# Optimization experiments

Hardware: AMD Instinct MI355X
Metric: run time of the kernel (lower is better)

The kernel has to match this reference:

```python
import jax, jax.numpy as jnp
import numpy as np


def setup_inputs() -> dict:
    key = jax.random.key(0)
    B, T, D, H = 64, 512, 1024, 1024
    ks = jax.random.split(key, 14)
    s = 1.0 / np.sqrt(D)  # torch nn.Linear init scale
    u = lambda k, shape: jax.random.uniform(k, shape, jnp.float32, -s, s)
    return {
        "x": jax.random.normal(ks[0], (B, T, D), jnp.float32),
        "h0": jnp.zeros((B, 1, H), jnp.float32),
        "Wfz": u(ks[1], (H, D)), "bfz": u(ks[2], (H,)),
        "Wfr": u(ks[3], (H, D)), "bfr": u(ks[4], (H,)),
        "Wfh": u(ks[5], (H, D)), "bfh": u(ks[6], (H,)),
        "Wuz": u(ks[7], (H, H)), "buz": u(ks[8], (H,)),
        "Wur": u(ks[9], (H, H)), "bur": u(ks[10], (H,)),
        "Wuh": u(ks[11], (H, H)), "buh": u(ks[12], (H,)),
        "chunk_size": 1,
    }


def reference(x, h0, Wfz, bfz, Wfr, bfr, Wfh, bfh, Wuz, buz, Wur, bur, Wuh, buh, chunk_size):
    # Input-side projections are time-independent: batch them over the whole
    # sequence (same math as applying fz/fr/fh per step).
    Xz = x @ Wfz.T + bfz  # [B,T,H]
    Xr = x @ Wfr.T + bfr
    Xh = x @ Wfh.T + bfh

    def step(h, xs):  # h: [B,H]
        xz, xr, xh = xs
        z = jax.nn.sigmoid(xz + h @ Wuz.T + buz)
        r = jax.nn.sigmoid(xr + h @ Wur.T + bur)
        h_hat = jax.nn.silu(xh + (r * h) @ Wuh.T + buh)
        h = (1.0 - z) * h + z * h_hat
        return h, h

    xs = (Xz.transpose(1, 0, 2), Xr.transpose(1, 0, 2), Xh.transpose(1, 0, 2))  # [T,B,H]
    h_last, ys = jax.lax.scan(step, h0[:, 0, :], xs)
    y = ys.transpose(1, 0, 2)  # [B,T,H]
    return y, h_last[:, None, :]
```

## Files before the change

### kernel.cpp

```cpp
#include <hip/hip_runtime.h>
#include <hip/hip_bf16.h>

typedef short s16x8 __attribute__((ext_vector_type(8)));
typedef float f32x4 __attribute__((ext_vector_type(4)));

__device__ __forceinline__ float bf2f(unsigned short s) {
  union { unsigned int u; float f; } c; c.u = ((unsigned int)s) << 16; return c.f;
}
__device__ __forceinline__ short f2bf(float f) {
  union { float f; unsigned int u; } c; c.f = f;
  unsigned int r = (c.u + 0x7fffu + ((c.u >> 16) & 1u)) >> 16;
  return (short)(unsigned short)r;
}
__device__ __forceinline__ float sigm(float x) { return 1.0f / (1.0f + __expf(-x)); }

__device__ __forceinline__ void gload_lds16(const short* g, short* l) {
  __builtin_amdgcn_global_load_lds((const __attribute__((address_space(1))) void*)g,
                                   (__attribute__((address_space(3))) void*)l, 16, 0, 0);
}

__device__ __forceinline__ void cload8(const short* p,
    s16x8& d0, s16x8& d1, s16x8& d2, s16x8& d3,
    s16x8& d4, s16x8& d5, s16x8& d6, s16x8& d7)
{
  asm volatile(
    "global_load_dwordx4 %0, %[p], off sc0 sc1\n\t"
    "global_load_dwordx4 %1, %[p], off offset:64 sc0 sc1\n\t"
    "global_load_dwordx4 %2, %[p], off offset:128 sc0 sc1\n\t"
    "global_load_dwordx4 %3, %[p], off offset:192 sc0 sc1\n\t"
    "global_load_dwordx4 %4, %[p], off offset:256 sc0 sc1\n\t"
    "global_load_dwordx4 %5, %[p], off offset:320 sc0 sc1\n\t"
    "global_load_dwordx4 %6, %[p], off offset:384 sc0 sc1\n\t"
    "global_load_dwordx4 %7, %[p], off offset:448 sc0 sc1"
    : "=&v"(d0), "=&v"(d1), "=&v"(d2), "=&v"(d3),
      "=&v"(d4), "=&v"(d5), "=&v"(d6), "=&v"(d7)
    : [p]"v"(p) : "memory");
}

__global__ void prep(const float* __restrict__ x,
                     const float* __restrict__ Wfz, const float* __restrict__ Wfr, const float* __restrict__ Wfh,
                     const float* __restrict__ Wuz, const float* __restrict__ Wur, const float* __restrict__ Wuh,
                     const float* __restrict__ h0,
                     short* __restrict__ xb, short* __restrict__ Wf, short* __restrict__ Wzr,
                     short* __restrict__ Wh, short* __restrict__ hb)
{
  const long NX = 33554432L;
  const long NW = 1048576L;
  const long TOT = NX + 6*NW + 65536L;
  long stride = (long)gridDim.x * blockDim.x;
  for (long p = (long)blockIdx.x * blockDim.x + threadIdx.x; p < TOT; p += stride) {
    if (p < NX) { xb[p] = f2bf(x[p]); }
    else if (p < NX + 3*NW) {
      long q = p - NX;
      float v = q < NW ? Wfz[q] : (q < 2*NW ? Wfr[q-NW] : Wfh[q-2*NW]);
      Wf[q] = f2bf(v);
    } else if (p < NX + 5*NW) {
      long q = p - NX - 3*NW;
      float v = q < NW ? Wuz[q] : Wur[q-NW];
      Wzr[q] = f2bf(v);
    } else if (p < NX + 6*NW) {
      long q = p - NX - 5*NW;
      Wh[q] = f2bf(Wuh[q]);
    } else {
      long q = p - NX - 6*NW;
      hb[q] = f2bf(h0[q]);
    }
  }
}

__global__ __launch_bounds__(256) void gemm_x(const short* __restrict__ A, const short* __restrict__ Bw,
    const float* __restrict__ bfz, const float* __restrict__ bfr, const float* __restrict__ bfh,
    short* __restrict__ X)
{
  constexpr int M = 32768, K = 1024;
  constexpr int BM = 128, BN = 128, BK = 32;
  __shared__ __align__(16) short As[BM*BK];
  __shared__ __align__(16) short Bs[BN*BK];
  int tid = threadIdx.x, lane = tid & 63, wid = tid >> 6;
  int bm = blockIdx.x % (M/BM), bn = blockIdx.x / (M/BM);
  int wm = wid >> 1, wn = wid & 1;

  f32x4 acc[4][4];
  for (int i = 0; i < 4; ++i) for (int j = 0; j < 4; ++j) acc[i][j] = f32x4{0.f,0.f,0.f,0.f};

  int r0 = tid >> 2,        kc0 = (tid & 3) * 8;
  int r1 = (256+tid) >> 2,  kc1 = ((256+tid) & 3) * 8;
  const short* a0 = A  + (size_t)(bm*BM + r0)*K + kc0;
  const short* a1 = A  + (size_t)(bm*BM + r1)*K + kc1;
  const short* b0 = Bw + (size_t)(bn*BN + r0)*K + kc0;
  const short* b1 = Bw + (size_t)(bn*BN + r1)*K + kc1;

  const short* abase = As + (wm*64 + (lane&15))*BK + (lane>>4)*8;
  const short* bbase = Bs + (wn*64 + (lane&15))*BK + (lane>>4)*8;

  for (int k0 = 0; k0 < K; k0 += BK) {
    __syncthreads();
    gload_lds16(a0 + k0, As + wid*512);
    gload_lds16(a1 + k0, As + 2048 + wid*512);
    gload_lds16(b0 + k0, Bs + wid*512);
    gload_lds16(b1 + k0, Bs + 2048 + wid*512);
    __syncthreads();
    s16x8 af[4], bff[4];
    for (int f = 0; f < 4; ++f) {
      af[f]  = *(const s16x8*)(abase + f*16*BK);
      bff[f] = *(const s16x8*)(bbase + f*16*BK);
    }
    for (int i = 0; i < 4; ++i)
      for (int j = 0; j < 4; ++j)
        acc[i][j] = __builtin_amdgcn_mfma_f32_16x16x32_bf16(af[i], bff[j], acc[i][j], 0, 0, 0);
  }

  int col = lane & 15, rb = (lane >> 4) * 4;
  for (int fi = 0; fi < 4; ++fi) for (int fj = 0; fj < 4; ++fj) {
    int n = bn*BN + wn*64 + fj*16 + col;
    float bias = n < 1024 ? bfz[n] : (n < 2048 ? bfr[n-1024] : bfh[n-2048]);
    f32x4 c = acc[fi][fj];
    for (int i = 0; i < 4; ++i) {
      int m = bm*BM + wm*64 + fi*16 + rb + i;
      int bb = m >> 9, tt = m & 511;
      X[((size_t)tt*64 + bb)*3072 + n] = f2bf(c[i] + bias);
    }
  }
}

#define WAITV(N) asm volatile("s_waitcnt vmcnt(" #N ")" ::: "memory"); \
                 __builtin_amdgcn_sched_barrier(0);

__global__ __launch_bounds__(64, 1) void recur(
  const short* __restrict__ X,
  const short* __restrict__ Wzr,
  const short* __restrict__ Wh,
  const float* __restrict__ h0,
  const float* __restrict__ buz, const float* __restrict__ bur, const float* __restrict__ buh,
  short* hb,
  short* rh,
  float* y, float* hlast, int* bar)
{
  __shared__ __align__(16) short Wl[3*32*64*8];

  int wg = blockIdx.x;
  int cg = wg & 63, bg = wg >> 6;
  int lane = threadIdx.x;
  int col = lane & 15, hi = lane >> 4;
  int rb = hi*4, kfo = hi*8;
  int j  = cg*16 + col;
  int b0 = bg*16 + rb;
  int arow = bg*16 + col;

  {
    const short* gbase0 = Wzr + (size_t)(cg*16 + col)*1024 + kfo;
    const short* gbase1 = Wzr + (size_t)(1024 + cg*16 + col)*1024 + kfo;
    const short* gbase2 = Wh  + (size_t)(cg*16 + col)*1024 + kfo;
    #pragma unroll 4
    for (int n = 0; n < 32; ++n) {
      *(s16x8*)(Wl + ((0*32+n)*64 + lane)*8) = *(const s16x8*)(gbase0 + n*32);
      *(s16x8*)(Wl + ((1*32+n)*64 + lane)*8) = *(const s16x8*)(gbase1 + n*32);
      *(s16x8*)(Wl + ((2*32+n)*64 + lane)*8) = *(const s16x8*)(gbase2 + n*32);
    }
  }

  float bz = buz[j], br = bur[j], bh = buh[j];
  float hreg[4], zreg[4];
  #pragma unroll
  for (int i = 0; i < 4; ++i) hreg[i] = h0[(b0+i)*1024 + j];

  unsigned short xs[12], xn[12];
  #pragma unroll
  for (int i = 0; i < 4; ++i) {
    const unsigned short* xp = (const unsigned short*)X + ((size_t)(b0+i))*3072 + j;
    xs[i] = xp[0]; xs[4+i] = xp[1024]; xs[8+i] = xp[2048];
  }

  const short* wlbase = Wl + lane*8;
  int* cnt = bar + bg*64;
  int tgt = 64;

  asm volatile("s_waitcnt vmcnt(0)" ::: "memory");

  for (int t = 0; t < 512; ++t) {
    const short* hbc = hb + (t&1)*65536;
    short* hbn = hb + ((t&1)^1)*65536;

    {
      const short* ap = hbc + (size_t)arow*1024 + kfo;
      s16x8 ah[32];
      cload8(ap,     ah[0], ah[1], ah[2], ah[3], ah[4], ah[5], ah[6], ah[7]);
      cload8(ap+256, ah[8], ah[9], ah[10],ah[11],ah[12],ah[13],ah[14],ah[15]);
      cload8(ap+512, ah[16],ah[17],ah[18],ah[19],ah[20],ah[21],ah[22],ah[23]);
      cload8(ap+768, ah[24],ah[25],ah[26],ah[27],ah[28],ah[29],ah[30],ah[31]);
      f32x4 acz = {0.f,0.f,0.f,0.f}, acr = {0.f,0.f,0.f,0.f};
      WAITV(24)
      #pragma unroll
      for (int n = 0; n < 8; ++n) {
        s16x8 vz = *(const s16x8*)(wlbase + n*512);
        s16x8 vr = *(const s16x8*)(wlbase + 16384 + n*512);
        acz = __builtin_amdgcn_mfma_f32_16x16x32_bf16(ah[n], vz, acz, 0,0,0);
        acr = __builtin_amdgcn_mfma_f32_16x16x32_bf16(ah[n], vr, acr, 0,0,0);
      }
      WAITV(16)
      #pragma unroll
      for (int n = 8; n < 16; ++n) {
        s16x8 vz = *(const s16x8*)(wlbase + n*512);
        s16x8 vr = *(const s16x8*)(wlbase + 16384 + n*512);
        acz = __builtin_amdgcn_mfma_f32_16x16x32_bf16(ah[n], vz, acz, 0,0,0);
        acr = __builtin_amdgcn_mfma_f32_16x16x32_bf16(ah[n], vr, acr, 0,0,0);
      }
      WAITV(8)
      #pragma unroll
      for (int n = 16; n < 24; ++n) {
        s16x8 vz = *(const s16x8*)(wlbase + n*512);
        s16x8 vr = *(const s16x8*)(wlbase + 16384 + n*512);
        acz = __builtin_amdgcn_mfma_f32_16x16x32_bf16(ah[n], vz, acz, 0,0,0);
        acr = __builtin_amdgcn_mfma_f32_16x16x32_bf16(ah[n], vr, acr, 0,0,0);
      }
      WAITV(0)
      #pragma unroll
      for (int n = 24; n < 32; ++n) {
        s16x8 vz = *(const s16x8*)(wlbase + n*512);
        s16x8 vr = *(const s16x8*)(wlbase + 16384 + n*512);
        acz = __builtin_amdgcn_mfma_f32_16x16x32_bf16(ah[n], vz, acz, 0,0,0);
        acr = __builtin_amdgcn_mfma_f32_16x16x32_bf16(ah[n], vr, acr, 0,0,0);
      }
      #pragma unroll
      for (int i = 0; i < 4; ++i) {
        zreg[i] = sigm(bf2f(xs[i]) + acz[i] + bz);
        float r = sigm(bf2f(xs[4+i]) + acr[i] + br);
        __hip_atomic_store(rh + (b0+i)*1024 + j, f2bf(r * hreg[i]),
                           __ATOMIC_RELAXED, __HIP_MEMORY_SCOPE_AGENT);
      }
    }
    asm volatile("s_waitcnt vmcnt(0)" ::: "memory");
    if (lane == 0)
      __hip_atomic_fetch_add(cnt, 1, __ATOMIC_RELAXED, __HIP_MEMORY_SCOPE_AGENT);
    {
      int v;
      do { v = __hip_atomic_load(cnt, __ATOMIC_RELAXED, __HIP_MEMORY_SCOPE_AGENT); }
      while (v < tgt);
      tgt += 64;
    }

    {
      const short* ap = rh + (size_t)arow*1024 + kfo;
      s16x8 ah[32];
      cload8(ap,     ah[0], ah[1], ah[2], ah[3], ah[4], ah[5], ah[6], ah[7]);
      cload8(ap+256, ah[8], ah[9], ah[10],ah[11],ah[12],ah[13],ah[14],ah[15]);
      cload8(ap+512, ah[16],ah[17],ah[18],ah[19],ah[20],ah[21],ah[22],ah[23]);
      cload8(ap+768, ah[24],ah[25],ah[26],ah[27],ah[28],ah[29],ah[30],ah[31]);
      f32x4 ach = {0.f,0.f,0.f,0.f};
      WAITV(24)
      #pragma unroll
      for (int n = 0; n < 8; ++n) {
        s16x8 vh = *(const s16x8*)(wlbase + 32768 + n*512);
        ach = __builtin_amdgcn_mfma_f32_16x16x32_bf16(ah[n], vh, ach, 0,0,0);
      }
      WAITV(16)
      #pragma unroll
      for (int n = 8; n < 16; ++n) {
        s16x8 vh = *(const s16x8*)(wlbase + 32768 + n*512);
        ach = __builtin_amdgcn_mfma_f32_16x16x32_bf16(ah[n], vh, ach, 0,0,0);
      }
      WAITV(8)
      #pragma unroll
      for (int n = 16; n < 24; ++n) {
        s16x8 vh = *(const s16x8*)(wlbase + 32768 + n*512);
        ach = __builtin_amdgcn_mfma_f32_16x16x32_bf16(ah[n], vh, ach, 0,0,0);
      }
      WAITV(0)
      #pragma unroll
      for (int n = 24; n < 32; ++n) {
        s16x8 vh = *(const s16x8*)(wlbase + 32768 + n*512);
        ach = __builtin_amdgcn_mfma_f32_16x16x32_bf16(ah[n], vh, ach, 0,0,0);
      }
      float hnv[4];
      #pragma unroll
      for (int i = 0; i < 4; ++i) {
        float s  = bf2f(xs[8+i]) + ach[i] + bh;
        float hh = s * sigm(s);
        float hn = (1.0f - zreg[i])*hreg[i] + zreg[i]*hh;
        hnv[i] = hn; hreg[i] = hn;
        __hip_atomic_store(hbn + (b0+i)*1024 + j, f2bf(hn),
                           __ATOMIC_RELAXED, __HIP_MEMORY_SCOPE_AGENT);
      }
      asm volatile("s_waitcnt vmcnt(0)" ::: "memory");
      if (lane == 0)
        __hip_atomic_fetch_add(cnt, 1, __ATOMIC_RELAXED, __HIP_MEMORY_SCOPE_AGENT);
      #pragma unroll
      for (int i = 0; i < 4; ++i)
        __builtin_nontemporal_store(hnv[i], y + ((size_t)(b0+i)*512 + t)*1024 + j);
      int tn = (t+1) & 511;
      #pragma unroll
      for (int i = 0; i < 4; ++i) {
        const unsigned short* xp = (const unsigned short*)X + ((size_t)tn*64 + (b0+i))*3072 + j;
        xn[i] = xp[0]; xn[4+i] = xp[1024]; xn[8+i] = xp[2048];
      }
      if (t == 511) {
        #pragma unroll
        for (int i = 0; i < 4; ++i) hlast[(b0+i)*1024 + j] = hreg[i];
      }
      {
        int v;
        do { v = __hip_atomic_load(cnt, __ATOMIC_RELAXED, __HIP_MEMORY_SCOPE_AGENT); }
        while (v < tgt);
        tgt += 64;
      }
    }

    #pragma unroll
    for (int q = 0; q < 12; ++q) xs[q] = xn[q];
  }
}

extern "C" void kernel_launch(void* const* d_in, const int* in_sizes, int n_in,
                              void* d_out, int out_size, void* d_ws, size_t ws_size,
                              hipStream_t stream) {
  const float* x   = (const float*)d_in[0];
  const float* h0  = (const float*)d_in[1];
  const float* Wfz = (const float*)d_in[2];
  const float* bfz = (const float*)d_in[3];
  const float* Wfr = (const float*)d_in[4];
  const float* bfr = (const float*)d_in[5];
  const float* Wfh = (const float*)d_in[6];
  const float* bfh = (const float*)d_in[7];
  const float* Wuz = (const float*)d_in[8];
  const float* buz = (const float*)d_in[9];
  const float* Wur = (const float*)d_in[10];
  const float* bur = (const float*)d_in[11];
  const float* Wuh = (const float*)d_in[12];
  const float* buh = (const float*)d_in[13];

  char* ws = (char*)d_ws;
  short* Xb  = (short*)(ws);
  short* xb  = (short*)(ws + 201326592);
  short* Wf  = (short*)(ws + 268435456);
  short* Wzr = (short*)(ws + 274726912);
  short* Wh  = (short*)(ws + 278921216);
  short* hb  = (short*)(ws + 281018368);
  short* rh  = (short*)(ws + 281280512);
  int*   bar = (int*)(ws + 281411584);

  float* y = (float*)d_out;
  float* hlast = y + 33554432;

  hipMemsetAsync(bar, 0, 1024, stream);
  prep<<<2048, 256, 0, stream>>>(x, Wfz, Wfr, Wfh, Wuz, Wur, Wuh, h0, xb, Wf, Wzr, Wh, hb);
  gemm_x<<<6144, 256, 0, stream>>>(xb, Wf, bfz, bfr, bfh, Xb);
  recur<<<256, 64, 0, stream>>>(Xb, Wzr, Wh, h0, buz, bur, buh, hb, rh, y, hlast, bar);
}
```

Before: 3.808 ms.

## Split recurrence into compute and helper waves, defer z-gate MFMAs past barrier

The recurrent kernel now runs two waves per block. A helper wave prefetches the X projections into LDS two steps ahead and writes y outputs from an LDS staging buffer, which takes global stores and loads off the critical wave. The compute wave computes r first, publishes r*h, and spreads the z-gate MFMAs across the grid barrier so they overlap the wait. It also uses split accumulators to shorten MFMA dependency chains and a multi-outstanding-load barrier poll. In exchange it adds intra-block flag handshakes that can stall the compute wave, plus extra ordering complexity.

```diff
diff --git a/kernel.cpp b/kernel.cpp
--- a/kernel.cpp
+++ b/kernel.cpp
@@ -18,6 +18,9 @@
   __builtin_amdgcn_global_load_lds((const __attribute__((address_space(1))) void*)g,
                                    (__attribute__((address_space(3))) void*)l, 16, 0, 0);
 }
+
+#define SB() __builtin_amdgcn_sched_barrier(0)
+#define WAITV(N) asm volatile("s_waitcnt vmcnt(" #N ")" ::: "memory"); SB();
 
 __device__ __forceinline__ void cload8(const short* p,
     s16x8& d0, s16x8& d1, s16x8& d2, s16x8& d3,
@@ -35,6 +38,38 @@
     : "=&v"(d0), "=&v"(d1), "=&v"(d2), "=&v"(d3),
       "=&v"(d4), "=&v"(d5), "=&v"(d6), "=&v"(d7)
     : [p]"v"(p) : "memory");
+}
+
+__device__ __forceinline__ void mgpoll(const int* cnt, int tgt) {
+  int t0, t1, t2, t3;
+  asm volatile(
+    "global_load_dword %0, %[a], off sc0 sc1\n\t"
+    "global_load_dword %1, %[a], off sc0 sc1\n\t"
+    "global_load_dword %2, %[a], off sc0 sc1\n\t"
+    "global_load_dword %3, %[a], off sc0 sc1\n"
+    "1:\n\t"
+    "s_waitcnt vmcnt(3)\n\t"
+    "v_cmp_ge_i32 vcc, %0, %[t]\n\t"
+    "s_cbranch_vccnz 2f\n\t"
+    "global_load_dword %0, %[a], off sc0 sc1\n\t"
+    "s_waitcnt vmcnt(3)\n\t"
+    "v_cmp_ge_i32 vcc, %1, %[t]\n\t"
+    "s_cbranch_vccnz 2f\n\t"
+    "global_load_dword %1, %[a], off sc0 sc1\n\t"
+    "s_waitcnt vmcnt(3)\n\t"
+    "v_cmp_ge_i32 vcc, %2, %[t]\n\t"
+    "s_cbranch_vccnz 2f\n\t"
+    "global_load_dword %2, %[a], off sc0 sc1\n\t"
+    "s_waitcnt vmcnt(3)\n\t"
+    "v_cmp_ge_i32 vcc, %3, %[t]\n\t"
+    "s_cbranch_vccnz 2f\n\t"
+    "global_load_dword %3, %[a], off sc0 sc1\n\t"
+    "s_branch 1b\n"
+    "2:\n\t"
+    "s_waitcnt vmcnt(0)"
+    : "=&v"(t0), "=&v"(t1), "=&v"(t2), "=&v"(t3)
+    : [a]"v"(cnt), [t]"v"(tgt)
+    : "vcc", "memory");
 }
 
 __global__ void prep(const float* __restrict__ x,
@@ -123,10 +158,9 @@
   }
 }
 
-#define WAITV(N) asm volatile("s_waitcnt vmcnt(" #N ")" ::: "memory"); \
-                 __builtin_amdgcn_sched_barrier(0);
-
-__global__ __launch_bounds__(64, 1) void recur(
+#define MFMA(a,b,c) __builtin_amdgcn_mfma_f32_16x16x32_bf16(a,b,c,0,0,0)
+
+__global__ __launch_bounds__(128, 1) void recur(
   const short* __restrict__ X,
   const short* __restrict__ Wzr,
   const short* __restrict__ Wh,
@@ -137,176 +171,202 @@
   float* y, float* hlast, int* bar)
 {
   __shared__ __align__(16) short Wl[3*32*64*8];
+  __shared__ __align__(16) unsigned short xls[2][12][64];
+  __shared__ __align__(16) float yls[2][4][64];
+  __shared__ int fl[4];
 
   int wg = blockIdx.x;
   int cg = wg & 63, bg = wg >> 6;
-  int lane = threadIdx.x;
+  int tid = threadIdx.x;
+  int lane = tid & 63, wv = tid >> 6;
   int col = lane & 15, hi = lane >> 4;
-  int rb = hi*4, kfo = hi*8;
+  int kfo = hi*8;
   int j  = cg*16 + col;
-  int b0 = bg*16 + rb;
+  int b0 = bg*16 + hi*4;
   int arow = bg*16 + col;
 
-  {
-    const short* gbase0 = Wzr + (size_t)(cg*16 + col)*1024 + kfo;
-    const short* gbase1 = Wzr + (size_t)(1024 + cg*16 + col)*1024 + kfo;
-    const short* gbase2 = Wh  + (size_t)(cg*16 + col)*1024 + kfo;
+  if (tid == 0) { fl[0]=0; fl[1]=0; fl[2]=0; fl[3]=0; }
+  __syncthreads();
+
+  if (wv == 0) {
+    const short* g0 = Wzr + (size_t)(cg*16+col)*1024 + kfo;
+    const short* g1 = Wzr + (size_t)(1024+cg*16+col)*1024 + kfo;
     #pragma unroll 4
     for (int n = 0; n < 32; ++n) {
-      *(s16x8*)(Wl + ((0*32+n)*64 + lane)*8) = *(const s16x8*)(gbase0 + n*32);
-      *(s16x8*)(Wl + ((1*32+n)*64 + lane)*8) = *(const s16x8*)(gbase1 + n*32);
-      *(s16x8*)(Wl + ((2*32+n)*64 + lane)*8) = *(const s16x8*)(gbase2 + n*32);
-    }
+      *(s16x8*)(Wl + (0*32+n)*512 + lane*8) = *(const s16x8*)(g0 + n*32);
+      *(s16x8*)(Wl + (1*32+n)*512 + lane*8) = *(const s16x8*)(g1 + n*32);
+    }
+  } else {
+    const short* g2 = Wh + (size_t)(cg*16+col)*1024 + kfo;
+    #pragma unroll 4
+    for (int n = 0; n < 32; ++n)
+      *(s16x8*)(Wl + (2*32+n)*512 + lane*8) = *(const s16x8*)(g2 + n*32);
+    for (int t = 0; t < 2; ++t)
+      for (int q = 0; q < 12; ++q)
+        xls[t][q][lane] = ((const unsigned short*)X)[((size_t)t*64 + b0 + (q&3))*3072 + (q>>2)*1024 + j];
+    if (lane == 0)
+      __hip_atomic_store(&fl[0], 2, __ATOMIC_RELEASE, __HIP_MEMORY_SCOPE_WORKGROUP);
   }
-
-  float bz = buz[j], br = bur[j], bh = buh[j];
-  float hreg[4], zreg[4];
-  #pragma unroll
-  for (int i = 0; i < 4; ++i) hreg[i] = h0[(b0+i)*1024 + j];
-
-  unsigned short xs[12], xn[12];
-  #pragma unroll
-  for (int i = 0; i < 4; ++i) {
-    const unsigned short* xp = (const unsigned short*)X + ((size_t)(b0+i))*3072 + j;
-    xs[i] = xp[0]; xs[4+i] = xp[1024]; xs[8+i] = xp[2048];
-  }
-
-  const short* wlbase = Wl + lane*8;
-  int* cnt = bar + bg*64;
-  int tgt = 64;
-
-  asm volatile("s_waitcnt vmcnt(0)" ::: "memory");
-
-  for (int t = 0; t < 512; ++t) {
-    const short* hbc = hb + (t&1)*65536;
-    short* hbn = hb + ((t&1)^1)*65536;
-
-    {
-      const short* ap = hbc + (size_t)arow*1024 + kfo;
-      s16x8 ah[32];
-      cload8(ap,     ah[0], ah[1], ah[2], ah[3], ah[4], ah[5], ah[6], ah[7]);
-      cload8(ap+256, ah[8], ah[9], ah[10],ah[11],ah[12],ah[13],ah[14],ah[15]);
-      cload8(ap+512, ah[16],ah[17],ah[18],ah[19],ah[20],ah[21],ah[22],ah[23]);
-      cload8(ap+768, ah[24],ah[25],ah[26],ah[27],ah[28],ah[29],ah[30],ah[31]);
-      f32x4 acz = {0.f,0.f,0.f,0.f}, acr = {0.f,0.f,0.f,0.f};
-      WAITV(24)
-      #pragma unroll
-      for (int n = 0; n < 8; ++n) {
-        s16x8 vz = *(const s16x8*)(wlbase + n*512);
-        s16x8 vr = *(const s16x8*)(wlbase + 16384 + n*512);
-        acz = __builtin_amdgcn_mfma_f32_16x16x32_bf16(ah[n], vz, acz, 0,0,0);
-        acr = __builtin_amdgcn_mfma_f32_16x16x32_bf16(ah[n], vr, acr, 0,0,0);
-      }
-      WAITV(16)
-      #pragma unroll
-      for (int n = 8; n < 16; ++n) {
-        s16x8 vz = *(const s16x8*)(wlbase + n*512);
-        s16x8 vr = *(const s16x8*)(wlbase + 16384 + n*512);
-        acz = __builtin_amdgcn_mfma_f32_16x16x32_bf16(ah[n], vz, acz, 0,0,0);
-        acr = __builtin_amdgcn_mfma_f32_16x16x32_bf16(ah[n], vr, acr, 0,0,0);
-      }
-      WAITV(8)
-      #pragma unroll
-      for (int n = 16; n < 24; ++n) {
-        s16x8 vz = *(const s16x8*)(wlbase + n*512);
-        s16x8 vr = *(const s16x8*)(wlbase + 16384 + n*512);
-        acz = __builtin_amdgcn_mfma_f32_16x16x32_bf16(ah[n], vz, acz, 0,0,0);
-        acr = __builtin_amdgcn_mfma_f32_16x16x32_bf16(ah[n], vr, acr, 0,0,0);
-      }
-      WAITV(0)
-      #pragma unroll
-      for (int n = 24; n < 32; ++n) {
-        s16x8 vz = *(const s16x8*)(wlbase + n*512);
-        s16x8 vr = *(const s16x8*)(wlbase + 16384 + n*512);
-        acz = __builtin_amdgcn_mfma_f32_16x16x32_bf16(ah[n], vz, acz, 0,0,0);
-        acr = __builtin_amdgcn_mfma_f32_16x16x32_bf16(ah[n], vr, acr, 0,0,0);
-      }
-      #pragma unroll
-      for (int i = 0; i < 4; ++i) {
-        zreg[i] = sigm(bf2f(xs[i]) + acz[i] + bz);
-        float r = sigm(bf2f(xs[4+i]) + acr[i] + br);
-        __hip_atomic_store(rh + (b0+i)*1024 + j, f2bf(r * hreg[i]),
-                           __ATOMIC_RELAXED, __HIP_MEMORY_SCOPE_AGENT);
-      }
-    }
+  __syncthreads();
+
+  if (wv == 0) {
+    float bz = buz[j], br = bur[j], bh = buh[j];
+    float hreg[4];
+    #pragma unroll
+    for (int i = 0; i < 4; ++i) hreg[i] = h0[(b0+i)*1024 + j];
+
+    const short* wlz = Wl + lane*8;
+    const short* wlr = Wl + 16384 + lane*8;
+    const short* wlh = Wl + 32768 + lane*8;
+    int* cnt = bar + bg*64;
+    int tgt = 64;
+
+    s16x8 ahh[32], ahr[32];
     asm volatile("s_waitcnt vmcnt(0)" ::: "memory");
-    if (lane == 0)
-      __hip_atomic_fetch_add(cnt, 1, __ATOMIC_RELAXED, __HIP_MEMORY_SCOPE_AGENT);
-    {
-      int v;
-      do { v = __hip_atomic_load(cnt, __ATOMIC_RELAXED, __HIP_MEMORY_SCOPE_AGENT); }
-      while (v < tgt);
-      tgt += 64;
-    }
-
-    {
-      const short* ap = rh + (size_t)arow*1024 + kfo;
-      s16x8 ah[32];
-      cload8(ap,     ah[0], ah[1], ah[2], ah[3], ah[4], ah[5], ah[6], ah[7]);
-      cload8(ap+256, ah[8], ah[9], ah[10],ah[11],ah[12],ah[13],ah[14],ah[15]);
-      cload8(ap+512, ah[16],ah[17],ah[18],ah[19],ah[20],ah[21],ah[22],ah[23]);
-      cload8(ap+768, ah[24],ah[25],ah[26],ah[27],ah[28],ah[29],ah[30],ah[31]);
-      f32x4 ach = {0.f,0.f,0.f,0.f};
-      WAITV(24)
-      #pragma unroll
-      for (int n = 0; n < 8; ++n) {
-        s16x8 vh = *(const s16x8*)(wlbase + 32768 + n*512);
-        ach = __builtin_amdgcn_mfma_f32_16x16x32_bf16(ah[n], vh, ach, 0,0,0);
-      }
-      WAITV(16)
-      #pragma unroll
-      for (int n = 8; n < 16; ++n) {
-        s16x8 vh = *(const s16x8*)(wlbase + 32768 + n*512);
-        ach = __builtin_amdgcn_mfma_f32_16x16x32_bf16(ah[n], vh, ach, 0,0,0);
-      }
-      WAITV(8)
-      #pragma unroll
-      for (int n = 16; n < 24; ++n) {
-        s16x8 vh = *(const s16x8*)(wlbase + 32768 + n*512);
-        ach = __builtin_amdgcn_mfma_f32_16x16x32_bf16(ah[n], vh, ach, 0,0,0);
-      }
-      WAITV(0)
-      #pragma unroll
-      for (int n = 24; n < 32; ++n) {
-        s16x8 vh = *(const s16x8*)(wlbase + 32768 + n*512);
-        ach = __builtin_amdgcn_mfma_f32_16x16x32_bf16(ah[n], vh, ach, 0,0,0);
-      }
-      float hnv[4];
-      #pragma unroll
-      for (int i = 0; i < 4; ++i) {
-        float s  = bf2f(xs[8+i]) + ach[i] + bh;
-        float hh = s * sigm(s);
-        float hn = (1.0f - zreg[i])*hreg[i] + zreg[i]*hh;
-        hnv[i] = hn; hreg[i] = hn;
-        __hip_atomic_store(hbn + (b0+i)*1024 + j, f2bf(hn),
-                           __ATOMIC_RELAXED, __HIP_MEMORY_SCOPE_AGENT);
+
+    for (int t = 0; t < 512; ++t) {
+      const short* hbc = hb + (t&1)*65536;
+      short* hbn = hb + ((t&1)^1)*65536;
+      f32x4 acz0 = {0.f,0.f,0.f,0.f}, acz1 = {0.f,0.f,0.f,0.f};
+      unsigned short xv[12];
+
+      {
+        const short* ap = hbc + (size_t)arow*1024 + kfo;
+        cload8(ap,     ahh[0], ahh[1], ahh[2], ahh[3], ahh[4], ahh[5], ahh[6], ahh[7]);
+        cload8(ap+256, ahh[8], ahh[9], ahh[10],ahh[11],ahh[12],ahh[13],ahh[14],ahh[15]);
+        cload8(ap+512, ahh[16],ahh[17],ahh[18],ahh[19],ahh[20],ahh[21],ahh[22],ahh[23]);
+        cload8(ap+768, ahh[24],ahh[25],ahh[26],ahh[27],ahh[28],ahh[29],ahh[30],ahh[31]);
+        SB();
+        while (__hip_atomic_load(&fl[0], __ATOMIC_ACQUIRE, __HIP_MEMORY_SCOPE_WORKGROUP) < t+1) {}
+        #pragma unroll
+        for (int q = 0; q < 12; ++q) xv[q] = xls[t&1][q][lane];
+        __hip_atomic_store(&fl[1], t+1, __ATOMIC_RELEASE, __HIP_MEMORY_SCOPE_WORKGROUP);
+
+        f32x4 acr0 = {0.f,0.f,0.f,0.f}, acr1 = {0.f,0.f,0.f,0.f};
+        WAITV(24)
+        #pragma unroll
+        for (int n = 0; n < 8; ++n) {
+          s16x8 w = *(const s16x8*)(wlr + n*512);
+          if (n&1) acr1 = MFMA(ahh[n], w, acr1); else acr0 = MFMA(ahh[n], w, acr0);
+        }
+        WAITV(16)
+        #pragma unroll
+        for (int n = 8; n < 16; ++n) {
+          s16x8 w = *(const s16x8*)(wlr + n*512);
+          if (n&1) acr1 = MFMA(ahh[n], w, acr1); else acr0 = MFMA(ahh[n], w, acr0);
+        }
+        WAITV(8)
+        #pragma unroll
+        for (int n = 16; n < 24; ++n) {
+          s16x8 w = *(const s16x8*)(wlr + n*512);
+          if (n&1) acr1 = MFMA(ahh[n], w, acr1); else acr0 = MFMA(ahh[n], w, acr0);
+        }
+        WAITV(0)
+        #pragma unroll
+        for (int n = 24; n < 32; ++n) {
+          s16x8 w = *(const s16x8*)(wlr + n*512);
+          if (n&1) acr1 = MFMA(ahh[n], w, acr1); else acr0 = MFMA(ahh[n], w, acr0);
+        }
+        #pragma unroll
+        for (int i = 0; i < 4; ++i) {
+          float r = sigm(bf2f(xv[4+i]) + acr0[i] + acr1[i] + br);
+          __hip_atomic_store(rh + (b0+i)*1024 + j, f2bf(r * hreg[i]),
+                             __ATOMIC_RELAXED, __HIP_MEMORY_SCOPE_AGENT);
+        }
+        SB();
+        #pragma unroll
+        for (int n = 0; n < 16; ++n) {
+          s16x8 w = *(const s16x8*)(wlz + n*512);
+          if (n&1) acz1 = MFMA(ahh[n], w, acz1); else acz0 = MFMA(ahh[n], w, acz0);
+        }
+        SB();
       }
       asm volatile("s_waitcnt vmcnt(0)" ::: "memory");
       if (lane == 0)
         __hip_atomic_fetch_add(cnt, 1, __ATOMIC_RELAXED, __HIP_MEMORY_SCOPE_AGENT);
+      mgpoll(cnt, tgt); tgt += 64;
+
+      {
+        const short* rp = rh + (size_t)arow*1024 + kfo;
+        cload8(rp,     ahr[0], ahr[1], ahr[2], ahr[3], ahr[4], ahr[5], ahr[6], ahr[7]);
+        cload8(rp+256, ahr[8], ahr[9], ahr[10],ahr[11],ahr[12],ahr[13],ahr[14],ahr[15]);
+        cload8(rp+512, ahr[16],ahr[17],ahr[18],ahr[19],ahr[20],ahr[21],ahr[22],ahr[23]);
+        cload8(rp+768, ahr[24],ahr[25],ahr[26],ahr[27],ahr[28],ahr[29],ahr[30],ahr[31]);
+        SB();
+        #pragma unroll
+        for (int n = 16; n < 32; ++n) {
+          s16x8 w = *(const s16x8*)(wlz + n*512);
+          if (n&1) acz1 = MFMA(ahh[n], w, acz1); else acz0 = MFMA(ahh[n], w, acz0);
+        }
+        f32x4 ach0 = {0.f,0.f,0.f,0.f}, ach1 = {0.f,0.f,0.f,0.f};
+        WAITV(24)
+        #pragma unroll
+        for (int n = 0; n < 8; ++n) {
+          s16x8 w = *(const s16x8*)(wlh + n*512);
+          if (n&1) ach1 = MFMA(ahr[n], w, ach1); else ach0 = MFMA(ahr[n], w, ach0);
+        }
+        WAITV(16)
+        #pragma unroll
+        for (int n = 8; n < 16; ++n) {
+          s16x8 w = *(const s16x8*)(wlh + n*512);
+          if (n&1) ach1 = MFMA(ahr[n], w, ach1); else ach0 = MFMA(ahr[n], w, ach0);
+        }
+        WAITV(8)
+        #pragma unroll
+        for (int n = 16; n < 24; ++n) {
+          s16x8 w = *(const s16x8*)(wlh + n*512);
+          if (n&1) ach1 = MFMA(ahr[n], w, ach1); else ach0 = MFMA(ahr[n], w, ach0);
+        }
+        WAITV(0)
+        #pragma unroll
+        for (int n = 24; n < 32; ++n) {
+          s16x8 w = *(const s16x8*)(wlh + n*512);
+          if (n&1) ach1 = MFMA(ahr[n], w, ach1); else ach0 = MFMA(ahr[n], w, ach0);
+        }
+        while (__hip_atomic_load(&fl[3], __ATOMIC_ACQUIRE, __HIP_MEMORY_SCOPE_WORKGROUP) < t-1) {}
+        #pragma unroll
+        for (int i = 0; i < 4; ++i) {
+          float z  = sigm(bf2f(xv[i]) + acz0[i] + acz1[i] + bz);
+          float s  = bf2f(xv[8+i]) + ach0[i] + ach1[i] + bh;
+          float hh = s * sigm(s);
+          float hn = (1.0f - z)*hreg[i] + z*hh;
+          hreg[i] = hn;
+          yls[t&1][i][lane] = hn;
+          __hip_atomic_store(hbn + (b0+i)*1024 + j, f2bf(hn),
+                             __ATOMIC_RELAXED, __HIP_MEMORY_SCOPE_AGENT);
+        }
+        __hip_atomic_store(&fl[2], t+1, __ATOMIC_RELEASE, __HIP_MEMORY_SCOPE_WORKGROUP);
+        SB();
+      }
+      asm volatile("s_waitcnt vmcnt(0)" ::: "memory");
+      if (lane == 0)
+        __hip_atomic_fetch_add(cnt, 1, __ATOMIC_RELAXED, __HIP_MEMORY_SCOPE_AGENT);
+      mgpoll(cnt, tgt); tgt += 64;
+    }
+    #pragma unroll
+    for (int i = 0; i < 4; ++i) hlast[(b0+i)*1024 + j] = hreg[i];
+  } else {
+    for (int t = 0; t < 512; ++t) {
+      while (__hip_atomic_load(&fl[2], __ATOMIC_ACQUIRE, __HIP_MEMORY_SCOPE_WORKGROUP) < t+1)
+        __builtin_amdgcn_s_sleep(2);
+      float yv[4];
       #pragma unroll
-      for (int i = 0; i < 4; ++i)
-        __builtin_nontemporal_store(hnv[i], y + ((size_t)(b0+i)*512 + t)*1024 + j);
-      int tn = (t+1) & 511;
+      for (int i = 0; i < 4; ++i) yv[i] = yls[t&1][i][lane];
       #pragma unroll
-      for (int i = 0; i < 4; ++i) {
-        const unsigned short* xp = (const unsigned short*)X + ((size_t)tn*64 + (b0+i))*3072 + j;
-        xn[i] = xp[0]; xn[4+i] = xp[1024]; xn[8+i] = xp[2048];
+      for (int i = 0; i < 4; ++i) y[((size_t)(b0+i)*512 + t)*1024 + j] = yv[i];
+      __hip_atomic_store(&fl[3], t+1, __ATOMIC_RELEASE, __HIP_MEMORY_SCOPE_WORKGROUP);
+      if (t + 2 < 512) {
+        while (__hip_atomic_load(&fl[1], __ATOMIC_ACQUIRE, __HIP_MEMORY_SCOPE_WORKGROUP) < t+1)
+          __builtin_amdgcn_s_sleep(2);
+        unsigned short xv[12];
+        #pragma unroll
+        for (int q = 0; q < 12; ++q)
+          xv[q] = ((const unsigned short*)X)[((size_t)(t+2)*64 + b0 + (q&3))*3072 + (q>>2)*1024 + j];
+        #pragma unroll
+        for (int q = 0; q < 12; ++q) xls[t&1][q][lane] = xv[q];
+        __hip_atomic_store(&fl[0], t+3, __ATOMIC_RELEASE, __HIP_MEMORY_SCOPE_WORKGROUP);
       }
-      if (t == 511) {
-        #pragma unroll
-        for (int i = 0; i < 4; ++i) hlast[(b0+i)*1024 + j] = hreg[i];
-      }
-      {
-        int v;
-        do { v = __hip_atomic_load(cnt, __ATOMIC_RELAXED, __HIP_MEMORY_SCOPE_AGENT); }
-        while (v < tgt);
-        tgt += 64;
-      }
-    }
-
-    #pragma unroll
-    for (int q = 0; q < 12; ++q) xs[q] = xn[q];
+    }
   }
 }
 
@@ -344,5 +404,5 @@
   hipMemsetAsync(bar, 0, 1024, stream);
   prep<<<2048, 256, 0, stream>>>(x, Wfz, Wfr, Wfh, Wuz, Wur, Wuh, h0, xb, Wf, Wzr, Wh, hb);
   gemm_x<<<6144, 256, 0, stream>>>(xb, Wf, bfz, bfr, bfh, Xb);
-  recur<<<256, 64, 0, stream>>>(Xb, Wzr, Wh, h0, buz, bur, buh, hb, rh, y, hlast, bar);
-}
+  recur<<<256, 128, 0, stream>>>(Xb, Wzr, Wh, h0, buz, bur, buh, hb, rh, y, hlast, bar);
+}
```

New measurement: 3.781 ms. No clear change (-0.7%).
